# Performance work log

Hardware: AMD Instinct MI355X
Metric: run time of the kernel (lower is better)

## Reference

```python
import jax, jax.numpy as jnp
import numpy as np

C_IN = 128
C_OUT = 128
P = 3
V = 4096
FIFO_SIZE = 17  # 2*kernel_size - 1, kernel_size = 9


def setup_inputs() -> dict:
    key = jax.random.key(0)
    k1, k2, k3, k4 = jax.random.split(key, 4)
    x = jax.random.normal(k1, (1, C_IN, V, 1), dtype=jnp.float32)
    A = jax.random.uniform(k2, (P, V, V), dtype=jnp.float32) / V  # roughly normalized adjacency
    fifo = jax.random.normal(k3, (FIFO_SIZE, P, C_OUT, V), dtype=jnp.float32)
    W = jax.random.normal(k4, (P * C_OUT, C_IN), dtype=jnp.float32) * 0.02  # 1x1 conv weight
    b = jnp.zeros((P * C_OUT,), dtype=jnp.float32)
    return {"x": x, "A": A, "fifo": fifo, "W": W, "b": b}


def reference(x, A, fifo, W, b):
    # x: (1, C_in, V, 1) single graph frame; residual = identity (C_in == C_out, stride 1)
    xv = x[0, :, :, 0]                                   # (C_in, V)
    # 1x1 conv -> split into P partitions: (P, C_out, V)
    z = (W @ xv + b[:, None]).reshape(P, C_OUT, V)
    # per-partition adjacency matmul: (P, C_out, V) @ (P, V, V)
    d = jnp.einsum('pcv,pvw->pcw', z, A)
    # FIFO push: newest frame in front, drop oldest
    new_fifo = jnp.concatenate([d[None], fifo[:FIFO_SIZE - 1]], axis=0)  # (FIFO, P, C_out, V)
    # temporal + partition reduction
    e = new_fifo.sum(axis=(0, 1))                        # (C_out, V)
    out = jax.nn.relu(e + xv)[None]                      # (1, C_out, V)
    return out
```

## Files before the change

kernel.cpp:

```cpp
#include <hip/hip_runtime.h>

typedef float f32x4 __attribute__((ext_vector_type(4)));
typedef __bf16 bf16x8 __attribute__((ext_vector_type(8)));

constexpr int V = 4096;

__device__ __forceinline__ unsigned short f2bf(float f) {
    unsigned int u = __float_as_uint(f);
    u += 0x7FFFu + ((u >> 16) & 1u);
    return (unsigned short)(u >> 16);
}

__global__ __launch_bounds__(256) void k_z(const float* __restrict__ x,
                                           const float* __restrict__ W,
                                           const float* __restrict__ b,
                                           unsigned short* __restrict__ zb) {
    __shared__ float Ws[8 * 128];
    __shared__ float bs[8];
    const int rg = blockIdx.x;
    const int vb = blockIdx.y;
    const int t  = threadIdx.x;
    reinterpret_cast<f32x4*>(Ws)[t] = reinterpret_cast<const f32x4*>(W + rg * 1024)[t];
    if (t < 8) bs[t] = b[rg * 8 + t];
    __syncthreads();
    const int v = vb * 256 + t;
    float acc[8] = {};
    for (int j = 0; j < 128; ++j) {
        const float xj = x[j * V + v];
        #pragma unroll
        for (int q = 0; q < 8; ++q) acc[q] = fmaf(Ws[q * 128 + j], xj, acc[q]);
    }
    #pragma unroll
    for (int q = 0; q < 8; ++q)
        zb[(size_t)(rg * 8 + q) * V + v] = f2bf(acc[q] + bs[q]);
}

__global__ __launch_bounds__(256) void k_gemm(const unsigned short* __restrict__ zb,
                                              const float* __restrict__ A,
                                              float* __restrict__ partial) {
    __shared__ unsigned short Bt[32][72];
    const int nt = blockIdx.x;
    const int p  = blockIdx.y;
    const int kh = blockIdx.z;
    const int n0 = nt * 32;
    const int kbase = kh * 2048;
    const int t    = threadIdx.x;
    const int wid  = t >> 6;
    const int lane = t & 63;
    const int lrow = lane & 15;
    const int g    = lane >> 4;

    const float* Ap = A + (size_t)p * V * V;
    const unsigned short* Zw = zb + ((size_t)p * 128 + wid * 32) * V;

    const int kk = t >> 2;
    const int c4 = t & 3;

    f32x4 acc00 = {}, acc01 = {}, acc10 = {}, acc11 = {};

    for (int k0 = kbase; k0 < kbase + 2048; k0 += 64) {
        const float* src = Ap + (size_t)(k0 + kk) * V + n0 + c4 * 4;
        f32x4 av0 = *reinterpret_cast<const f32x4*>(src);
        f32x4 av1 = *reinterpret_cast<const f32x4*>(src + 16);
        __syncthreads();
        #pragma unroll
        for (int j = 0; j < 4; ++j) {
            Bt[c4 * 4 + j][kk]      = f2bf(av0[j]);
            Bt[16 + c4 * 4 + j][kk] = f2bf(av1[j]);
        }
        __syncthreads();
        const unsigned short* zrow = Zw + (size_t)lrow * V + k0 + g * 8;
        #pragma unroll
        for (int ks = 0; ks < 2; ++ks) {
            bf16x8 b0 = *reinterpret_cast<const bf16x8*>(&Bt[lrow][ks * 32 + g * 8]);
            bf16x8 b1 = *reinterpret_cast<const bf16x8*>(&Bt[16 + lrow][ks * 32 + g * 8]);
            bf16x8 a0 = *reinterpret_cast<const bf16x8*>(zrow + ks * 32);
            bf16x8 a1 = *reinterpret_cast<const bf16x8*>(zrow + (size_t)16 * V + ks * 32);
            acc00 = __builtin_amdgcn_mfma_f32_16x16x32_bf16(a0, b0, acc00, 0, 0, 0);
            acc01 = __builtin_amdgcn_mfma_f32_16x16x32_bf16(a0, b1, acc01, 0, 0, 0);
            acc10 = __builtin_amdgcn_mfma_f32_16x16x32_bf16(a1, b0, acc10, 0, 0, 0);
            acc11 = __builtin_amdgcn_mfma_f32_16x16x32_bf16(a1, b1, acc11, 0, 0, 0);
        }
    }

    float* Pp = partial + (size_t)(p * 2 + kh) * 128 * V;
    #pragma unroll
    for (int r = 0; r < 4; ++r) {
        const int m0 = wid * 32 + g * 4 + r;
        Pp[(size_t)m0 * V + n0 + lrow]             = acc00[r];
        Pp[(size_t)m0 * V + n0 + 16 + lrow]        = acc01[r];
        Pp[(size_t)(m0 + 16) * V + n0 + lrow]      = acc10[r];
        Pp[(size_t)(m0 + 16) * V + n0 + 16 + lrow] = acc11[r];
    }
}

__global__ __launch_bounds__(256) void k_epi(const float* __restrict__ x,
                                             const float* __restrict__ fifo,
                                             const float* __restrict__ partial,
                                             float* __restrict__ out) {
    const size_t off  = ((size_t)blockIdx.x * 256 + threadIdx.x) * 4;
    const size_t slab = (size_t)128 * V;
    f32x4 s0 = *reinterpret_cast<const f32x4*>(x + off);
    f32x4 s1 = {}, s2 = {}, s3 = {};
    #pragma unroll
    for (int q = 0; q < 6; ++q) {
        f32x4 pv = *reinterpret_cast<const f32x4*>(partial + (size_t)q * slab + off);
        if (q & 1) s1 += pv; else s2 += pv;
    }
    #pragma unroll
    for (int s = 0; s < 48; ++s) {
        f32x4 fv = *reinterpret_cast<const f32x4*>(fifo + (size_t)s * slab + off);
        switch (s & 3) {
            case 0: s0 += fv; break;
            case 1: s1 += fv; break;
            case 2: s2 += fv; break;
            default: s3 += fv; break;
        }
    }
    f32x4 sum = (s0 + s1) + (s2 + s3);
    f32x4 o;
    #pragma unroll
    for (int j = 0; j < 4; ++j) o[j] = fmaxf(sum[j], 0.0f);
    *reinterpret_cast<f32x4*>(out + off) = o;
}

extern "C" void kernel_launch(void* const* d_in, const int* in_sizes, int n_in,
                              void* d_out, int out_size, void* d_ws, size_t ws_size,
                              hipStream_t stream) {
    const float* x    = (const float*)d_in[0];
    const float* A    = (const float*)d_in[1];
    const float* fifo = (const float*)d_in[2];
    const float* W    = (const float*)d_in[3];
    const float* b    = (const float*)d_in[4];
    float* out = (float*)d_out;

    unsigned short* zb = (unsigned short*)d_ws;
    float* partial = (float*)((char*)d_ws + (size_t)384 * V * 2);

    k_z   <<<dim3(48, 16),   256, 0, stream>>>(x, W, b, zb);
    k_gemm<<<dim3(128, 3, 2), 256, 0, stream>>>(zb, A, partial);
    k_epi <<<dim3(512),       256, 0, stream>>>(x, fifo, partial, out);
}
```

Baseline: 104.9 us.

## Prefetch A tiles, split K four ways, store bf16 partials, vectorize z kernel

```diff
diff --git a/kernel.cpp b/kernel.cpp
--- a/kernel.cpp
+++ b/kernel.cpp
@@ -2,13 +2,20 @@
 
 typedef float f32x4 __attribute__((ext_vector_type(4)));
 typedef __bf16 bf16x8 __attribute__((ext_vector_type(8)));
+typedef unsigned short u16x4 __attribute__((ext_vector_type(4)));
 
 constexpr int V = 4096;
+constexpr int KSPLIT = 4;
+constexpr int KSLAB  = V / KSPLIT;
+constexpr int NSLAB  = 3 * KSPLIT;
 
 __device__ __forceinline__ unsigned short f2bf(float f) {
     unsigned int u = __float_as_uint(f);
     u += 0x7FFFu + ((u >> 16) & 1u);
     return (unsigned short)(u >> 16);
+}
+__device__ __forceinline__ float bf2f(unsigned short h) {
+    return __uint_as_float(((unsigned int)h) << 16);
 }
 
 __global__ __launch_bounds__(256) void k_z(const float* __restrict__ x,
@@ -23,27 +30,32 @@
     reinterpret_cast<f32x4*>(Ws)[t] = reinterpret_cast<const f32x4*>(W + rg * 1024)[t];
     if (t < 8) bs[t] = b[rg * 8 + t];
     __syncthreads();
-    const int v = vb * 256 + t;
-    float acc[8] = {};
+    const int v = vb * 1024 + t * 4;
+    f32x4 acc[8] = {};
+    #pragma unroll 8
     for (int j = 0; j < 128; ++j) {
-        const float xj = x[j * V + v];
+        f32x4 xv = *reinterpret_cast<const f32x4*>(x + (size_t)j * V + v);
         #pragma unroll
-        for (int q = 0; q < 8; ++q) acc[q] = fmaf(Ws[q * 128 + j], xj, acc[q]);
+        for (int q = 0; q < 8; ++q) acc[q] += Ws[q * 128 + j] * xv;
     }
     #pragma unroll
-    for (int q = 0; q < 8; ++q)
-        zb[(size_t)(rg * 8 + q) * V + v] = f2bf(acc[q] + bs[q]);
+    for (int q = 0; q < 8; ++q) {
+        u16x4 u;
+        #pragma unroll
+        for (int j = 0; j < 4; ++j) u[j] = f2bf(acc[q][j] + bs[q]);
+        *reinterpret_cast<u16x4*>(zb + (size_t)(rg * 8 + q) * V + v) = u;
+    }
 }
 
 __global__ __launch_bounds__(256) void k_gemm(const unsigned short* __restrict__ zb,
                                               const float* __restrict__ A,
-                                              float* __restrict__ partial) {
+                                              unsigned short* __restrict__ partial) {
     __shared__ unsigned short Bt[32][72];
     const int nt = blockIdx.x;
     const int p  = blockIdx.y;
     const int kh = blockIdx.z;
     const int n0 = nt * 32;
-    const int kbase = kh * 2048;
+    const int kbase = kh * KSLAB, kend = kbase + KSLAB;
     const int t    = threadIdx.x;
     const int wid  = t >> 6;
     const int lane = t & 63;
@@ -57,16 +69,25 @@
     const int c4 = t & 3;
 
     f32x4 acc00 = {}, acc01 = {}, acc10 = {}, acc11 = {};
+    f32x4 av0, av1;
+    {
+        const float* src = Ap + (size_t)(kbase + kk) * V + n0 + c4 * 4;
+        av0 = *reinterpret_cast<const f32x4*>(src);
+        av1 = *reinterpret_cast<const f32x4*>(src + 16);
+    }
 
-    for (int k0 = kbase; k0 < kbase + 2048; k0 += 64) {
-        const float* src = Ap + (size_t)(k0 + kk) * V + n0 + c4 * 4;
-        f32x4 av0 = *reinterpret_cast<const f32x4*>(src);
-        f32x4 av1 = *reinterpret_cast<const f32x4*>(src + 16);
+    for (int k0 = kbase; k0 < kend; k0 += 64) {
         __syncthreads();
         #pragma unroll
         for (int j = 0; j < 4; ++j) {
             Bt[c4 * 4 + j][kk]      = f2bf(av0[j]);
             Bt[16 + c4 * 4 + j][kk] = f2bf(av1[j]);
+        }
+        {
+            const int kn = (k0 + 64 < kend) ? k0 + 64 : kbase;
+            const float* src = Ap + (size_t)(kn + kk) * V + n0 + c4 * 4;
+            av0 = *reinterpret_cast<const f32x4*>(src);
+            av1 = *reinterpret_cast<const f32x4*>(src + 16);
         }
         __syncthreads();
         const unsigned short* zrow = Zw + (size_t)lrow * V + k0 + g * 8;
@@ -83,30 +104,25 @@
         }
     }
 
-    float* Pp = partial + (size_t)(p * 2 + kh) * 128 * V;
+    unsigned short* Pp = partial + (size_t)(p * KSPLIT + kh) * 128 * V;
     #pragma unroll
     for (int r = 0; r < 4; ++r) {
         const int m0 = wid * 32 + g * 4 + r;
-        Pp[(size_t)m0 * V + n0 + lrow]             = acc00[r];
-        Pp[(size_t)m0 * V + n0 + 16 + lrow]        = acc01[r];
-        Pp[(size_t)(m0 + 16) * V + n0 + lrow]      = acc10[r];
-        Pp[(size_t)(m0 + 16) * V + n0 + 16 + lrow] = acc11[r];
+        Pp[(size_t)m0 * V + n0 + lrow]             = f2bf(acc00[r]);
+        Pp[(size_t)m0 * V + n0 + 16 + lrow]        = f2bf(acc01[r]);
+        Pp[(size_t)(m0 + 16) * V + n0 + lrow]      = f2bf(acc10[r]);
+        Pp[(size_t)(m0 + 16) * V + n0 + 16 + lrow] = f2bf(acc11[r]);
     }
 }
 
 __global__ __launch_bounds__(256) void k_epi(const float* __restrict__ x,
                                              const float* __restrict__ fifo,
-                                             const float* __restrict__ partial,
+                                             const unsigned short* __restrict__ partial,
                                              float* __restrict__ out) {
     const size_t off  = ((size_t)blockIdx.x * 256 + threadIdx.x) * 4;
     const size_t slab = (size_t)128 * V;
     f32x4 s0 = *reinterpret_cast<const f32x4*>(x + off);
     f32x4 s1 = {}, s2 = {}, s3 = {};
-    #pragma unroll
-    for (int q = 0; q < 6; ++q) {
-        f32x4 pv = *reinterpret_cast<const f32x4*>(partial + (size_t)q * slab + off);
-        if (q & 1) s1 += pv; else s2 += pv;
-    }
     #pragma unroll
     for (int s = 0; s < 48; ++s) {
         f32x4 fv = *reinterpret_cast<const f32x4*>(fifo + (size_t)s * slab + off);
@@ -116,6 +132,14 @@
             case 2: s2 += fv; break;
             default: s3 += fv; break;
         }
+    }
+    #pragma unroll
+    for (int q = 0; q < NSLAB; ++q) {
+        u16x4 pv = *reinterpret_cast<const u16x4*>(partial + (size_t)q * slab + off);
+        f32x4 d;
+        #pragma unroll
+        for (int j = 0; j < 4; ++j) d[j] = bf2f(pv[j]);
+        if (q & 1) s1 += d; else s2 += d;
     }
     f32x4 sum = (s0 + s1) + (s2 + s3);
     f32x4 o;
@@ -134,10 +158,10 @@
     const float* b    = (const float*)d_in[4];
     float* out = (float*)d_out;
 
-    unsigned short* zb = (unsigned short*)d_ws;
-    float* partial = (float*)((char*)d_ws + (size_t)384 * V * 2);
+    unsigned short* zb      = (unsigned short*)d_ws;
+    unsigned short* partial = (unsigned short*)((char*)d_ws + (size_t)3 * 1024 * 1024);
 
-    k_z   <<<dim3(48, 16),   256, 0, stream>>>(x, W, b, zb);
-    k_gemm<<<dim3(128, 3, 2), 256, 0, stream>>>(zb, A, partial);
-    k_epi <<<dim3(512),       256, 0, stream>>>(x, fifo, partial, out);
+    k_z   <<<dim3(48, 4),          256, 0, stream>>>(x, W, b, zb);
+    k_gemm<<<dim3(128, 3, KSPLIT), 256, 0, stream>>>(zb, A, partial);
+    k_epi <<<dim3(512),            256, 0, stream>>>(x, fifo, partial, out);
 }
```

Result: slower. 118.4 us (+12.9%).
